# Kernel optimization log

Hardware: AMD Instinct MI355X
Metric: run time of the kernel (lower is better)

The kernel has to match this reference:

```python
import jax, jax.numpy as jnp
import numpy as np

IN = (8, 8, 8, 8)
OUT = (8, 8, 8, 8)
RANK = (1, 16, 16, 16, 1)  # boundary ranks = 1
BATCH = 4096


def setup_inputs() -> dict:
    key = jax.random.key(0)
    ks = jax.random.split(key, 5)
    x = jax.random.normal(ks[0], (BATCH, int(np.prod(IN))), dtype=jnp.float32)
    scale = 0.7  # matches nn.init.uniform_(f, -0.7, 0.7)
    factors = {}
    for k in range(4):
        shp = (RANK[k], OUT[k], IN[k], RANK[k + 1])
        factors[f"f{k}"] = jax.random.uniform(ks[k + 1], shp, jnp.float32, -scale, scale)
    bias = jnp.zeros((int(np.prod(OUT)),), dtype=jnp.float32)  # init.constant_(bias, 0)
    return {"x": x, **factors, "bias": bias}


def reference(x, f0, f1, f2, f3, bias):
    """TT-matrix linear: y = TT(W) @ x_vec + bias, cores of shape (r1, o, i, r2)."""
    cores = [f0, f1, f2, f3]
    B = x.shape[0]
    i0 = cores[0].shape[2]
    # t: (B, A=accumulated out dims, r=current rank, i=current in dim, X=remaining in dims)
    t = x.reshape(B, 1, 1, i0, -1)
    n = len(cores)
    for k, c in enumerate(cores):
        r1, o, i, r2 = c.shape
        # contract current rank and current input mode
        t = jnp.einsum('barix,rois->baosx', t, c)
        A = t.shape[1] * t.shape[2]
        X = t.shape[4]
        if k + 1 < n:
            i_next = cores[k + 1].shape[2]
            t = t.reshape(B, A, r2, i_next, X // i_next)
        else:
            t = t.reshape(B, A)  # r2 == 1, X == 1
    return t + bias
```

## Files before the change

kernel.cpp:

```cpp
#include <hip/hip_runtime.h>

typedef unsigned short u16;
typedef unsigned int u32;
typedef __attribute__((ext_vector_type(8))) short bf16x8;
typedef __attribute__((ext_vector_type(4))) float f32x4;

__device__ __forceinline__ u16 f2bf(float f) {
  u32 u = __float_as_uint(f);
  u += 0x7fffu + ((u >> 16) & 1u);
  return (u16)(u >> 16);
}

__global__ void prep_small(const float* __restrict__ f0, const float* __restrict__ f1,
                           const float* __restrict__ f2, const float* __restrict__ f3,
                           float* __restrict__ W01, float* __restrict__ W23) {
  int b = blockIdx.x;
  if (b < 256) {
    int idx = b * 256 + threadIdx.x;
    int r2 = idx & 15; int t = idx >> 4;
    int i1 = t & 7; t >>= 3;
    int i0 = t & 7; t >>= 3;
    int o1 = t & 7; int o0 = t >> 3;
    const float* a = f0 + (o0 * 8 + i0) * 16;
    const float* c = f1 + (o1 * 8 + i1) * 16 + r2;
    float s = 0.f;
#pragma unroll
    for (int r1 = 0; r1 < 16; ++r1) s += a[r1] * c[r1 * 1024];
    W01[idx] = s;
  } else {
    int idx = (b - 256) * 256 + threadIdx.x;
    int i3 = idx & 7, o3 = (idx >> 3) & 7, i2 = (idx >> 6) & 7;
    int o2 = (idx >> 9) & 7, r2 = idx >> 12;
    const float* a = f2 + ((r2 * 8 + o2) * 8 + i2) * 16;
    const float* c = f3 + o3 * 8 + i3;
    float s = 0.f;
#pragma unroll
    for (int r3 = 0; r3 < 16; ++r3) s += a[r3] * c[r3 * 64];
    W23[idx] = s;
  }
}

__global__ void prep_big(const float* __restrict__ W01, const float* __restrict__ W23,
                         const float* __restrict__ x, u16* __restrict__ W,
                         uint4* __restrict__ xb) {
  int b = blockIdx.x;
  if (b < 8192) {
    int idx = b * 256 + threadIdx.x;
    float4 a = ((const float4*)x)[idx * 2], d = ((const float4*)x)[idx * 2 + 1];
    union { u16 h[8]; uint4 v; } r;
    r.h[0] = f2bf(a.x); r.h[1] = f2bf(a.y); r.h[2] = f2bf(a.z); r.h[3] = f2bf(a.w);
    r.h[4] = f2bf(d.x); r.h[5] = f2bf(d.y); r.h[6] = f2bf(d.z); r.h[7] = f2bf(d.w);
    xb[idx] = r.v;
    return;
  }
  const int o = b - 8192;
  const int o2 = (o >> 3) & 7, o3 = o & 7;
  const int tid = threadIdx.x;
  __shared__ float sW23[1024];

  {
    int e = tid * 4;
    const float* src = W23 + (e >> 6) * 4096 + o2 * 512 + ((e >> 3) & 7) * 64
                         + o3 * 8 + (e & 7);
    ((float4*)sW23)[tid] = *(const float4*)src;
  }
  float w01r[16];
  {
    const float* a = W01 + (((o >> 6) * 64 + (tid >> 2)) << 4);
#pragma unroll
    for (int q = 0; q < 4; ++q) {
      float4 v = *(const float4*)(a + q * 4);
      w01r[q * 4] = v.x; w01r[q * 4 + 1] = v.y; w01r[q * 4 + 2] = v.z; w01r[q * 4 + 3] = v.w;
    }
  }
  __syncthreads();

  const int i2a = 2 * (tid & 3), i2b = i2a + 1;
  float acc[16] = {};
#pragma unroll
  for (int r2 = 0; r2 < 16; ++r2) {
    const float w = w01r[r2];
    const float4 va0 = *(const float4*)(sW23 + r2 * 64 + i2a * 8);
    const float4 va1 = *(const float4*)(sW23 + r2 * 64 + i2a * 8 + 4);
    const float4 vb0 = *(const float4*)(sW23 + r2 * 64 + i2b * 8);
    const float4 vb1 = *(const float4*)(sW23 + r2 * 64 + i2b * 8 + 4);
    acc[0]  += w * va0.x; acc[1]  += w * va0.y; acc[2]  += w * va0.z; acc[3]  += w * va0.w;
    acc[4]  += w * va1.x; acc[5]  += w * va1.y; acc[6]  += w * va1.z; acc[7]  += w * va1.w;
    acc[8]  += w * vb0.x; acc[9]  += w * vb0.y; acc[10] += w * vb0.z; acc[11] += w * vb0.w;
    acc[12] += w * vb1.x; acc[13] += w * vb1.y; acc[14] += w * vb1.z; acc[15] += w * vb1.w;
  }
  union { u16 h[8]; uint4 v; } r0, r1;
#pragma unroll
  for (int j = 0; j < 8; ++j) { r0.h[j] = f2bf(acc[j]); r1.h[j] = f2bf(acc[8 + j]); }
  uint4* dst = (uint4*)(W + (size_t)o * 4096 + tid * 16);
  dst[0] = r0.v; dst[1] = r1.v;
}

__device__ __forceinline__ void gload_lds16(const void* g, void* l) {
  __builtin_amdgcn_global_load_lds((__attribute__((address_space(1))) void*)(g),
                                   (__attribute__((address_space(3))) void*)(l),
                                   16, 0, 0);
}

__global__ __launch_bounds__(512, 2) void gemm256(
    const u16* __restrict__ A, const u16* __restrict__ B,
    const float* __restrict__ bias, float* __restrict__ C) {
  constexpr int K = 4096, N = 4096, NT = 128;
  __shared__ u16 S[65536];
  const int tid  = threadIdx.x;
  const int wave = tid >> 6, lane = tid & 63;
  const int l15 = lane & 15, l4 = lane >> 4;
  const int wr = wave >> 2, wc = wave & 3;
  const int bm = (int)(blockIdx.x >> 4) * 256;
  const int bn = (int)(blockIdx.x & 15) * 256;

  const int rl = tid >> 2;
  const int ls = (tid & 3) ^ ((rl >> 1) & 3);
  const u16* srcA0 = A + (size_t)(bm +       rl) * K + ls * 8;
  const u16* srcA1 = A + (size_t)(bm + 128 + rl) * K + ls * 8;
  const u16* srcB0 = B + (size_t)(bn +       rl) * K + ls * 8;
  const u16* srcB1 = B + (size_t)(bn + 128 + rl) * K + ls * 8;
  const int dA0 = wave * 512,         dA1 = 4096  + wave * 512;
  const int dB0 = 8192 + wave * 512,  dB1 = 12288 + wave * 512;

  int offA[8], offB[4];
#pragma unroll
  for (int mi = 0; mi < 8; ++mi) {
    int r = wr * 128 + mi * 16 + l15;
    offA[mi] = r * 32 + ((l4 ^ ((r >> 1) & 3)) * 8);
  }
#pragma unroll
  for (int ni = 0; ni < 4; ++ni) {
    int r = wc * 64 + ni * 16 + l15;
    offB[ni] = 8192 + r * 32 + ((l4 ^ ((r >> 1) & 3)) * 8);
  }

#define STAGE_A(kts) do { int _s = (kts) & 3; u16* _b = S + _s * 16384;          \
    gload_lds16(srcA0 + (size_t)(kts) * 32, _b + dA0);                           \
    gload_lds16(srcA1 + (size_t)(kts) * 32, _b + dA1); } while (0)
#define STAGE_B(kts) do { int _s = (kts) & 3; u16* _b = S + _s * 16384;          \
    gload_lds16(srcB0 + (size_t)(kts) * 32, _b + dB0);                           \
    gload_lds16(srcB1 + (size_t)(kts) * 32, _b + dB1); } while (0)

  STAGE_A(0); STAGE_B(0);
  STAGE_A(1); STAGE_B(1);
  STAGE_A(2); STAGE_B(2);
  asm volatile("s_waitcnt vmcnt(8)" ::: "memory");
  __builtin_amdgcn_s_barrier();

  f32x4 acc[8][4] = {};

  for (int kt = 0; kt < NT; ++kt) {
    const u16* base = S + (kt & 3) * 16384;
    const int kn = (kt + 3) & (NT - 1);

    bf16x8 av[4], bv[4];
#pragma unroll
    for (int i = 0; i < 4; ++i) av[i] = *(const bf16x8*)(base + offA[i]);
#pragma unroll
    for (int i = 0; i < 4; ++i) bv[i] = *(const bf16x8*)(base + offB[i]);
    STAGE_A(kn);
    __builtin_amdgcn_s_barrier();
    __builtin_amdgcn_s_setprio(1);
#pragma unroll
    for (int mi = 0; mi < 4; ++mi)
#pragma unroll
      for (int ni = 0; ni < 4; ++ni)
        acc[mi][ni] = __builtin_amdgcn_mfma_f32_16x16x32_bf16(
            av[mi], bv[ni], acc[mi][ni], 0, 0, 0);
    __builtin_amdgcn_s_setprio(0);
    __builtin_amdgcn_s_barrier();

#pragma unroll
    for (int i = 0; i < 4; ++i) av[i] = *(const bf16x8*)(base + offA[4 + i]);
    STAGE_B(kn);
    asm volatile("s_waitcnt vmcnt(8)" ::: "memory");
    __builtin_amdgcn_s_barrier();
    __builtin_amdgcn_s_setprio(1);
#pragma unroll
    for (int mi = 0; mi < 4; ++mi)
#pragma unroll
      for (int ni = 0; ni < 4; ++ni)
        acc[4 + mi][ni] = __builtin_amdgcn_mfma_f32_16x16x32_bf16(
            av[mi], bv[ni], acc[4 + mi][ni], 0, 0, 0);
    __builtin_amdgcn_s_setprio(0);
    __builtin_amdgcn_s_barrier();
  }

#pragma unroll
  for (int ni = 0; ni < 4; ++ni) {
    const int col = bn + wc * 64 + ni * 16 + l15;
    const float bvs = bias[col];
#pragma unroll
    for (int mi = 0; mi < 8; ++mi) {
      const int row0 = bm + wr * 128 + mi * 16 + l4 * 4;
#pragma unroll
      for (int j = 0; j < 4; ++j)
        C[(size_t)(row0 + j) * N + col] = acc[mi][ni][j] + bvs;
    }
  }
  asm volatile("s_waitcnt vmcnt(0)" ::: "memory");
#undef STAGE_A
#undef STAGE_B
}

extern "C" void kernel_launch(void* const* d_in, const int* in_sizes, int n_in,
                              void* d_out, int out_size, void* d_ws, size_t ws_size,
                              hipStream_t stream) {
  const float* x    = (const float*)d_in[0];
  const float* f0   = (const float*)d_in[1];
  const float* f1   = (const float*)d_in[2];
  const float* f2   = (const float*)d_in[3];
  const float* f3   = (const float*)d_in[4];
  const float* bias = (const float*)d_in[5];

  char* ws = (char*)d_ws;
  u16* Wb = (u16*)(ws);
  u16* xb = (u16*)(ws + 33554432);
  float* W01 = (float*)d_out;
  float* W23 = (float*)d_out + 65536;

  prep_small<<<512,   256, 0, stream>>>(f0, f1, f2, f3, W01, W23);
  prep_big  <<<12288, 256, 0, stream>>>(W01, W23, x, Wb, (uint4*)xb);
  gemm256   <<<256,   512, 0, stream>>>(xb, Wb, bias, (float*)d_out);
}
```

Measured before the change: 153.9 us.

## Software-pipeline LDS fragment loads across k-tiles in the bf16 GEMM main loop

The GEMM main loop is unrolled by two and uses ping-pong B-fragment registers. The A and B fragments for the next k-tile are read from LDS during the second half of the current tile's MFMAs. This cuts the block barriers per k-tile from four to two and hides LDS read latency behind matrix work. It adds sched_barrier fences around the waitcnt, and the extra fragment registers raise VGPR pressure under launch_bounds(512,2).

```diff
diff --git a/kernel.cpp b/kernel.cpp
--- a/kernel.cpp
+++ b/kernel.cpp
@@ -57,7 +57,6 @@
   const int o2 = (o >> 3) & 7, o3 = o & 7;
   const int tid = threadIdx.x;
   __shared__ float sW23[1024];
-
   {
     int e = tid * 4;
     const float* src = W23 + (e >> 6) * 4096 + o2 * 512 + ((e >> 3) & 7) * 64
@@ -142,49 +141,61 @@
     gload_lds16(srcB0 + (size_t)(kts) * 32, _b + dB0);                           \
     gload_lds16(srcB1 + (size_t)(kts) * 32, _b + dB1); } while (0)
 
+#define ITER(kt, bvU, bvL)                                                       \
+  {                                                                              \
+    const u16* base  = S + ((kt) & 3) * 16384;                                   \
+    const u16* baseN = S + (((kt) + 1) & 3) * 16384;                             \
+    const int kn = ((kt) + 3) & (NT - 1);                                        \
+        \
+    bf16x8 avN[4];                                                               \
+    _Pragma("unroll")                                                            \
+    for (int i = 0; i < 4; ++i) avN[i] = *(const bf16x8*)(base + offA[4 + i]);   \
+    STAGE_A(kn);                                                                 \
+    __builtin_amdgcn_s_setprio(1);                                               \
+    _Pragma("unroll")                                                            \
+    for (int mi = 0; mi < 4; ++mi)                                               \
+      _Pragma("unroll")                                                          \
+      for (int ni = 0; ni < 4; ++ni)                                             \
+        acc[mi][ni] = __builtin_amdgcn_mfma_f32_16x16x32_bf16(                   \
+            avC[mi], bvU[ni], acc[mi][ni], 0, 0, 0);                             \
+    __builtin_amdgcn_s_setprio(0);                                               \
+      \
+    STAGE_B(kn);                                                                 \
+    asm volatile("s_waitcnt vmcnt(8)" ::: "memory");                             \
+    __builtin_amdgcn_sched_barrier(0);                                           \
+    __builtin_amdgcn_s_barrier();                                                \
+    _Pragma("unroll")                                                            \
+    for (int i = 0; i < 4; ++i) avC[i] = *(const bf16x8*)(baseN + offA[i]);      \
+    _Pragma("unroll")                                                            \
+    for (int i = 0; i < 4; ++i) bvL[i] = *(const bf16x8*)(baseN + offB[i]);      \
+    __builtin_amdgcn_s_setprio(1);                                               \
+    _Pragma("unroll")                                                            \
+    for (int mi = 0; mi < 4; ++mi)                                               \
+      _Pragma("unroll")                                                          \
+      for (int ni = 0; ni < 4; ++ni)                                             \
+        acc[4 + mi][ni] = __builtin_amdgcn_mfma_f32_16x16x32_bf16(               \
+            avN[mi], bvU[ni], acc[4 + mi][ni], 0, 0, 0);                         \
+    __builtin_amdgcn_s_setprio(0);                                               \
+    __builtin_amdgcn_s_barrier();                                                \
+  }
+
   STAGE_A(0); STAGE_B(0);
   STAGE_A(1); STAGE_B(1);
   STAGE_A(2); STAGE_B(2);
   asm volatile("s_waitcnt vmcnt(8)" ::: "memory");
+  __builtin_amdgcn_sched_barrier(0);
   __builtin_amdgcn_s_barrier();
 
   f32x4 acc[8][4] = {};
-
-  for (int kt = 0; kt < NT; ++kt) {
-    const u16* base = S + (kt & 3) * 16384;
-    const int kn = (kt + 3) & (NT - 1);
-
-    bf16x8 av[4], bv[4];
-#pragma unroll
-    for (int i = 0; i < 4; ++i) av[i] = *(const bf16x8*)(base + offA[i]);
-#pragma unroll
-    for (int i = 0; i < 4; ++i) bv[i] = *(const bf16x8*)(base + offB[i]);
-    STAGE_A(kn);
-    __builtin_amdgcn_s_barrier();
-    __builtin_amdgcn_s_setprio(1);
-#pragma unroll
-    for (int mi = 0; mi < 4; ++mi)
-#pragma unroll
-      for (int ni = 0; ni < 4; ++ni)
-        acc[mi][ni] = __builtin_amdgcn_mfma_f32_16x16x32_bf16(
-            av[mi], bv[ni], acc[mi][ni], 0, 0, 0);
-    __builtin_amdgcn_s_setprio(0);
-    __builtin_amdgcn_s_barrier();
-
-#pragma unroll
-    for (int i = 0; i < 4; ++i) av[i] = *(const bf16x8*)(base + offA[4 + i]);
-    STAGE_B(kn);
-    asm volatile("s_waitcnt vmcnt(8)" ::: "memory");
-    __builtin_amdgcn_s_barrier();
-    __builtin_amdgcn_s_setprio(1);
-#pragma unroll
-    for (int mi = 0; mi < 4; ++mi)
-#pragma unroll
-      for (int ni = 0; ni < 4; ++ni)
-        acc[4 + mi][ni] = __builtin_amdgcn_mfma_f32_16x16x32_bf16(
-            av[mi], bv[ni], acc[4 + mi][ni], 0, 0, 0);
-    __builtin_amdgcn_s_setprio(0);
-    __builtin_amdgcn_s_barrier();
+  bf16x8 avC[4], bvE[4], bvO[4];
+#pragma unroll
+  for (int i = 0; i < 4; ++i) avC[i] = *(const bf16x8*)(S + offA[i]);
+#pragma unroll
+  for (int i = 0; i < 4; ++i) bvE[i] = *(const bf16x8*)(S + offB[i]);
+
+  for (int kt = 0; kt < NT; kt += 2) {
+    ITER(kt,     bvE, bvO)
+    ITER(kt + 1, bvO, bvE)
   }
 
 #pragma unroll
@@ -202,6 +213,7 @@
   asm volatile("s_waitcnt vmcnt(0)" ::: "memory");
 #undef STAGE_A
 #undef STAGE_B
+#undef ITER
 }
 
 extern "C" void kernel_launch(void* const* d_in, const int* in_sizes, int n_in,
```

Measured after the change: 148.6 us. -3.4%, faster.

## Use 4-wave 128x128 per-wave tiles with register double-buffered LDS fragments

Applied to the files above, without the earlier changes.

The GEMM block drops from 8 waves to 4 waves, and each wave now computes a 128x128 output tile (8x8 MFMA accumulators) instead of 128x64. Each thread issues four staged load groups per k-step. The next k-step's A and B fragments are prefetched from LDS into registers while the current MFMAs run, removing one barrier pair and the setprio toggles. The aim is more MFMA work per LDS read and better overlap of LDS reads with compute. The cost is much higher register pressure (256 accumulator floats per lane) and fewer waves available to hide latency.

```diff
diff --git a/kernel.cpp b/kernel.cpp
--- a/kernel.cpp
+++ b/kernel.cpp
@@ -57,7 +57,6 @@
   const int o2 = (o >> 3) & 7, o3 = o & 7;
   const int tid = threadIdx.x;
   __shared__ float sW23[1024];
-
   {
     int e = tid * 4;
     const float* src = W23 + (e >> 6) * 4096 + o2 * 512 + ((e >> 3) & 7) * 64
@@ -102,7 +101,7 @@
                                    16, 0, 0);
 }
 
-__global__ __launch_bounds__(512, 2) void gemm256(
+__global__ __launch_bounds__(256, 1) void gemm256(
     const u16* __restrict__ A, const u16* __restrict__ B,
     const float* __restrict__ bias, float* __restrict__ C) {
   constexpr int K = 4096, N = 4096, NT = 128;
@@ -110,86 +109,113 @@
   const int tid  = threadIdx.x;
   const int wave = tid >> 6, lane = tid & 63;
   const int l15 = lane & 15, l4 = lane >> 4;
-  const int wr = wave >> 2, wc = wave & 3;
+  const int wr = wave >> 1, wc = wave & 1;
   const int bm = (int)(blockIdx.x >> 4) * 256;
   const int bn = (int)(blockIdx.x & 15) * 256;
 
-  const int rl = tid >> 2;
-  const int ls = (tid & 3) ^ ((rl >> 1) & 3);
-  const u16* srcA0 = A + (size_t)(bm +       rl) * K + ls * 8;
-  const u16* srcA1 = A + (size_t)(bm + 128 + rl) * K + ls * 8;
-  const u16* srcB0 = B + (size_t)(bn +       rl) * K + ls * 8;
-  const u16* srcB1 = B + (size_t)(bn + 128 + rl) * K + ls * 8;
-  const int dA0 = wave * 512,         dA1 = 4096  + wave * 512;
-  const int dB0 = 8192 + wave * 512,  dB1 = 12288 + wave * 512;
-
-  int offA[8], offB[4];
+  const int rg = tid >> 2;
+  const int ls = (tid & 3) ^ ((rg >> 1) & 3);
+  const u16* pA0 = A + (size_t)(bm +       rg) * K + ls * 8;
+  const u16* pA1 = A + (size_t)(bm +  64 + rg) * K + ls * 8;
+  const u16* pA2 = A + (size_t)(bm + 128 + rg) * K + ls * 8;
+  const u16* pA3 = A + (size_t)(bm + 192 + rg) * K + ls * 8;
+  const u16* pB0 = B + (size_t)(bn +       rg) * K + ls * 8;
+  const u16* pB1 = B + (size_t)(bn +  64 + rg) * K + ls * 8;
+  const u16* pB2 = B + (size_t)(bn + 128 + rg) * K + ls * 8;
+  const u16* pB3 = B + (size_t)(bn + 192 + rg) * K + ls * 8;
+  const int dl = tid * 8;
+
+  int offA[8], offB[8];
 #pragma unroll
   for (int mi = 0; mi < 8; ++mi) {
     int r = wr * 128 + mi * 16 + l15;
     offA[mi] = r * 32 + ((l4 ^ ((r >> 1) & 3)) * 8);
   }
 #pragma unroll
-  for (int ni = 0; ni < 4; ++ni) {
-    int r = wc * 64 + ni * 16 + l15;
+  for (int ni = 0; ni < 8; ++ni) {
+    int r = wc * 128 + ni * 16 + l15;
     offB[ni] = 8192 + r * 32 + ((l4 ^ ((r >> 1) & 3)) * 8);
   }
 
-#define STAGE_A(kts) do { int _s = (kts) & 3; u16* _b = S + _s * 16384;          \
-    gload_lds16(srcA0 + (size_t)(kts) * 32, _b + dA0);                           \
-    gload_lds16(srcA1 + (size_t)(kts) * 32, _b + dA1); } while (0)
-#define STAGE_B(kts) do { int _s = (kts) & 3; u16* _b = S + _s * 16384;          \
-    gload_lds16(srcB0 + (size_t)(kts) * 32, _b + dB0);                           \
-    gload_lds16(srcB1 + (size_t)(kts) * 32, _b + dB1); } while (0)
-
-  STAGE_A(0); STAGE_B(0);
-  STAGE_A(1); STAGE_B(1);
-  STAGE_A(2); STAGE_B(2);
-  asm volatile("s_waitcnt vmcnt(8)" ::: "memory");
+#define STG_A01(kts) do { u16* _b = S + ((kts) & 3) * 16384;                     \
+    gload_lds16(pA0 + (size_t)(kts) * 32, _b + dl);                              \
+    gload_lds16(pA1 + (size_t)(kts) * 32, _b + 2048 + dl); } while (0)
+#define STG_A23(kts) do { u16* _b = S + ((kts) & 3) * 16384;                     \
+    gload_lds16(pA2 + (size_t)(kts) * 32, _b + 4096 + dl);                       \
+    gload_lds16(pA3 + (size_t)(kts) * 32, _b + 6144 + dl); } while (0)
+#define STG_B01(kts) do { u16* _b = S + ((kts) & 3) * 16384;                     \
+    gload_lds16(pB0 + (size_t)(kts) * 32, _b + 8192 + dl);                       \
+    gload_lds16(pB1 + (size_t)(kts) * 32, _b + 10240 + dl); } while (0)
+#define STG_B23(kts) do { u16* _b = S + ((kts) & 3) * 16384;                     \
+    gload_lds16(pB2 + (size_t)(kts) * 32, _b + 12288 + dl);                      \
+    gload_lds16(pB3 + (size_t)(kts) * 32, _b + 14336 + dl); } while (0)
+#define STAGE_ALL(kts) do { STG_A01(kts); STG_A23(kts); STG_B01(kts); STG_B23(kts); } while (0)
+
+  STAGE_ALL(0); STAGE_ALL(1); STAGE_ALL(2);
+  asm volatile("s_waitcnt vmcnt(16)" ::: "memory");
+  __builtin_amdgcn_sched_barrier(0);
   __builtin_amdgcn_s_barrier();
 
-  f32x4 acc[8][4] = {};
+  f32x4 acc[8][8] = {};
+  bf16x8 a0[4], a1[4], b0[4], b1[4];
+#pragma unroll
+  for (int i = 0; i < 4; ++i) a0[i] = *(const bf16x8*)(S + offA[i]);
+#pragma unroll
+  for (int i = 0; i < 4; ++i) b0[i] = *(const bf16x8*)(S + offB[i]);
 
   for (int kt = 0; kt < NT; ++kt) {
-    const u16* base = S + (kt & 3) * 16384;
+    const u16* base  = S + (kt & 3) * 16384;
+    const u16* baseN = S + ((kt + 1) & 3) * 16384;
     const int kn = (kt + 3) & (NT - 1);
 
-    bf16x8 av[4], bv[4];
-#pragma unroll
-    for (int i = 0; i < 4; ++i) av[i] = *(const bf16x8*)(base + offA[i]);
-#pragma unroll
-    for (int i = 0; i < 4; ++i) bv[i] = *(const bf16x8*)(base + offB[i]);
-    STAGE_A(kn);
+#pragma unroll
+    for (int i = 0; i < 4; ++i) a1[i] = *(const bf16x8*)(base + offA[4 + i]);
+    STG_A01(kn);
+#pragma unroll
+    for (int mi = 0; mi < 4; ++mi)
+#pragma unroll
+      for (int ni = 0; ni < 4; ++ni)
+        acc[mi][ni] = __builtin_amdgcn_mfma_f32_16x16x32_bf16(
+            a0[mi], b0[ni], acc[mi][ni], 0, 0, 0);
+
+#pragma unroll
+    for (int i = 0; i < 4; ++i) b1[i] = *(const bf16x8*)(base + offB[4 + i]);
+    STG_A23(kn);
+#pragma unroll
+    for (int mi = 0; mi < 4; ++mi)
+#pragma unroll
+      for (int ni = 0; ni < 4; ++ni)
+        acc[4 + mi][ni] = __builtin_amdgcn_mfma_f32_16x16x32_bf16(
+            a1[mi], b0[ni], acc[4 + mi][ni], 0, 0, 0);
+    asm volatile("s_waitcnt vmcnt(12)" ::: "memory");
+    __builtin_amdgcn_sched_barrier(0);
     __builtin_amdgcn_s_barrier();
-    __builtin_amdgcn_s_setprio(1);
-#pragma unroll
-    for (int mi = 0; mi < 4; ++mi)
-#pragma unroll
-      for (int ni = 0; ni < 4; ++ni)
-        acc[mi][ni] = __builtin_amdgcn_mfma_f32_16x16x32_bf16(
-            av[mi], bv[ni], acc[mi][ni], 0, 0, 0);
-    __builtin_amdgcn_s_setprio(0);
+
+#pragma unroll
+    for (int i = 0; i < 4; ++i) b0[i] = *(const bf16x8*)(baseN + offB[i]);
+    STG_B01(kn);
+#pragma unroll
+    for (int mi = 0; mi < 4; ++mi)
+#pragma unroll
+      for (int ni = 0; ni < 4; ++ni)
+        acc[mi][4 + ni] = __builtin_amdgcn_mfma_f32_16x16x32_bf16(
+            a0[mi], b1[ni], acc[mi][4 + ni], 0, 0, 0);
+
+#pragma unroll
+    for (int i = 0; i < 4; ++i) a0[i] = *(const bf16x8*)(baseN + offA[i]);
+    STG_B23(kn);
+#pragma unroll
+    for (int mi = 0; mi < 4; ++mi)
+#pragma unroll
+      for (int ni = 0; ni < 4; ++ni)
+        acc[4 + mi][4 + ni] = __builtin_amdgcn_mfma_f32_16x16x32_bf16(
+            a1[mi], b1[ni], acc[4 + mi][4 + ni], 0, 0, 0);
     __builtin_amdgcn_s_barrier();
-
-#pragma unroll
-    for (int i = 0; i < 4; ++i) av[i] = *(const bf16x8*)(base + offA[4 + i]);
-    STAGE_B(kn);
-    asm volatile("s_waitcnt vmcnt(8)" ::: "memory");
-    __builtin_amdgcn_s_barrier();
-    __builtin_amdgcn_s_setprio(1);
-#pragma unroll
-    for (int mi = 0; mi < 4; ++mi)
-#pragma unroll
-      for (int ni = 0; ni < 4; ++ni)
-        acc[4 + mi][ni] = __builtin_amdgcn_mfma_f32_16x16x32_bf16(
-            av[mi], bv[ni], acc[4 + mi][ni], 0, 0, 0);
-    __builtin_amdgcn_s_setprio(0);
-    __builtin_amdgcn_s_barrier();
-  }
-
-#pragma unroll
-  for (int ni = 0; ni < 4; ++ni) {
-    const int col = bn + wc * 64 + ni * 16 + l15;
+  }
+
+#pragma unroll
+  for (int ni = 0; ni < 8; ++ni) {
+    const int col = bn + wc * 128 + ni * 16 + l15;
     const float bvs = bias[col];
 #pragma unroll
     for (int mi = 0; mi < 8; ++mi) {
@@ -200,8 +226,11 @@
     }
   }
   asm volatile("s_waitcnt vmcnt(0)" ::: "memory");
-#undef STAGE_A
-#undef STAGE_B
+#undef STG_A01
+#undef STG_A23
+#undef STG_B01
+#undef STG_B23
+#undef STAGE_ALL
 }
 
 extern "C" void kernel_launch(void* const* d_in, const int* in_sizes, int n_in,
@@ -222,5 +251,5 @@
 
   prep_small<<<512,   256, 0, stream>>>(f0, f1, f2, f3, W01, W23);
   prep_big  <<<12288, 256, 0, stream>>>(W01, W23, x, Wb, (uint4*)xb);
-  gemm256   <<<256,   512, 0, stream>>>(xb, Wb, bias, (float*)d_out);
-}
+  gemm256   <<<256,   256, 0, stream>>>(xb, Wb, bias, (float*)d_out);
+}
```

Result: slower. 370.9 us (+141.0%).

## Retile GEMM to 256x128 tiles with 4 waves and double-buffered LDS

Applied to the files above, without the earlier changes.

Changes the GEMM block from 512 threads on 256x256 tiles to 256 threads on 256x128 tiles, doubling the grid to 512 blocks. The 4-stage split A/B pipeline becomes a 2-slot double buffer with one combined stage per k-step, and sched_group_barrier hints interleave LDS reads, MFMAs and global loads. It cuts barriers per iteration and shrinks LDS so more blocks can be resident, but it waits on vmcnt(0) every iteration and each block reads more A data relative to its output.

```diff
diff --git a/kernel.cpp b/kernel.cpp
--- a/kernel.cpp
+++ b/kernel.cpp
@@ -57,7 +57,6 @@
   const int o2 = (o >> 3) & 7, o3 = o & 7;
   const int tid = threadIdx.x;
   __shared__ float sW23[1024];
-
   {
     int e = tid * 4;
     const float* src = W23 + (e >> 6) * 4096 + o2 * 512 + ((e >> 3) & 7) * 64
@@ -102,26 +101,27 @@
                                    16, 0, 0);
 }
 
-__global__ __launch_bounds__(512, 2) void gemm256(
+__global__ __launch_bounds__(256, 2) void gemm256(
     const u16* __restrict__ A, const u16* __restrict__ B,
     const float* __restrict__ bias, float* __restrict__ C) {
   constexpr int K = 4096, N = 4096, NT = 128;
-  __shared__ u16 S[65536];
+  __shared__ u16 S[24576];
   const int tid  = threadIdx.x;
   const int wave = tid >> 6, lane = tid & 63;
   const int l15 = lane & 15, l4 = lane >> 4;
-  const int wr = wave >> 2, wc = wave & 3;
-  const int bm = (int)(blockIdx.x >> 4) * 256;
-  const int bn = (int)(blockIdx.x & 15) * 256;
-
-  const int rl = tid >> 2;
-  const int ls = (tid & 3) ^ ((rl >> 1) & 3);
-  const u16* srcA0 = A + (size_t)(bm +       rl) * K + ls * 8;
-  const u16* srcA1 = A + (size_t)(bm + 128 + rl) * K + ls * 8;
-  const u16* srcB0 = B + (size_t)(bn +       rl) * K + ls * 8;
-  const u16* srcB1 = B + (size_t)(bn + 128 + rl) * K + ls * 8;
-  const int dA0 = wave * 512,         dA1 = 4096  + wave * 512;
-  const int dB0 = 8192 + wave * 512,  dB1 = 12288 + wave * 512;
+  const int wr = wave >> 1, wc = wave & 1;
+  const int bm = (int)(blockIdx.x >> 5) * 256;
+  const int bn = (int)(blockIdx.x & 31) * 128;
+
+  const int ls = (tid & 3) ^ ((tid >> 3) & 3);
+  const int rr = tid >> 2;
+  const u16* srcA0 = A + (size_t)(bm +       rr) * K + ls * 8;
+  const u16* srcA1 = A + (size_t)(bm +  64 + rr) * K + ls * 8;
+  const u16* srcA2 = A + (size_t)(bm + 128 + rr) * K + ls * 8;
+  const u16* srcA3 = A + (size_t)(bm + 192 + rr) * K + ls * 8;
+  const u16* srcB0 = B + (size_t)(bn +       rr) * K + ls * 8;
+  const u16* srcB1 = B + (size_t)(bn +  64 + rr) * K + ls * 8;
+  const int d8 = tid * 8;
 
   int offA[8], offB[4];
 #pragma unroll
@@ -135,55 +135,53 @@
     offB[ni] = 8192 + r * 32 + ((l4 ^ ((r >> 1) & 3)) * 8);
   }
 
-#define STAGE_A(kts) do { int _s = (kts) & 3; u16* _b = S + _s * 16384;          \
-    gload_lds16(srcA0 + (size_t)(kts) * 32, _b + dA0);                           \
-    gload_lds16(srcA1 + (size_t)(kts) * 32, _b + dA1); } while (0)
-#define STAGE_B(kts) do { int _s = (kts) & 3; u16* _b = S + _s * 16384;          \
-    gload_lds16(srcB0 + (size_t)(kts) * 32, _b + dB0);                           \
-    gload_lds16(srcB1 + (size_t)(kts) * 32, _b + dB1); } while (0)
-
-  STAGE_A(0); STAGE_B(0);
-  STAGE_A(1); STAGE_B(1);
-  STAGE_A(2); STAGE_B(2);
-  asm volatile("s_waitcnt vmcnt(8)" ::: "memory");
+#define STAGE(kts, slot) do { u16* _b = S + (slot) * 12288;                      \
+    gload_lds16(srcA0 + (size_t)(kts) * 32, _b + d8);                            \
+    gload_lds16(srcA1 + (size_t)(kts) * 32, _b + 2048 + d8);                     \
+    gload_lds16(srcA2 + (size_t)(kts) * 32, _b + 4096 + d8);                     \
+    gload_lds16(srcA3 + (size_t)(kts) * 32, _b + 6144 + d8);                     \
+    gload_lds16(srcB0 + (size_t)(kts) * 32, _b + 8192 + d8);                     \
+    gload_lds16(srcB1 + (size_t)(kts) * 32, _b + 10240 + d8); } while (0)
+
+  STAGE(0, 0);
+  asm volatile("s_waitcnt vmcnt(0)");
   __builtin_amdgcn_s_barrier();
 
   f32x4 acc[8][4] = {};
 
   for (int kt = 0; kt < NT; ++kt) {
-    const u16* base = S + (kt & 3) * 16384;
-    const int kn = (kt + 3) & (NT - 1);
-
-    bf16x8 av[4], bv[4];
-#pragma unroll
-    for (int i = 0; i < 4; ++i) av[i] = *(const bf16x8*)(base + offA[i]);
-#pragma unroll
-    for (int i = 0; i < 4; ++i) bv[i] = *(const bf16x8*)(base + offB[i]);
-    STAGE_A(kn);
-    __builtin_amdgcn_s_barrier();
-    __builtin_amdgcn_s_setprio(1);
+    const u16* base = S + (kt & 1) * 12288;
+
+    bf16x8 av[4], avN[4], bv[4];
+#pragma unroll
+    for (int i = 0; i < 4; ++i) av[i]  = *(const bf16x8*)(base + offA[i]);
+#pragma unroll
+    for (int i = 0; i < 4; ++i) bv[i]  = *(const bf16x8*)(base + offB[i]);
+#pragma unroll
+    for (int i = 0; i < 4; ++i) avN[i] = *(const bf16x8*)(base + offA[4 + i]);
+    STAGE((kt + 1) & (NT - 1), (kt & 1) ^ 1);
+
 #pragma unroll
     for (int mi = 0; mi < 4; ++mi)
 #pragma unroll
       for (int ni = 0; ni < 4; ++ni)
         acc[mi][ni] = __builtin_amdgcn_mfma_f32_16x16x32_bf16(
             av[mi], bv[ni], acc[mi][ni], 0, 0, 0);
-    __builtin_amdgcn_s_setprio(0);
-    __builtin_amdgcn_s_barrier();
-
-#pragma unroll
-    for (int i = 0; i < 4; ++i) av[i] = *(const bf16x8*)(base + offA[4 + i]);
-    STAGE_B(kn);
-    asm volatile("s_waitcnt vmcnt(8)" ::: "memory");
-    __builtin_amdgcn_s_barrier();
-    __builtin_amdgcn_s_setprio(1);
 #pragma unroll
     for (int mi = 0; mi < 4; ++mi)
 #pragma unroll
       for (int ni = 0; ni < 4; ++ni)
         acc[4 + mi][ni] = __builtin_amdgcn_mfma_f32_16x16x32_bf16(
-            av[mi], bv[ni], acc[4 + mi][ni], 0, 0, 0);
-    __builtin_amdgcn_s_setprio(0);
+            avN[mi], bv[ni], acc[4 + mi][ni], 0, 0, 0);
+
+    __builtin_amdgcn_sched_group_barrier(0x100, 8, 0);
+    __builtin_amdgcn_sched_group_barrier(0x008, 4, 0);
+    __builtin_amdgcn_sched_group_barrier(0x100, 4, 0);
+    __builtin_amdgcn_sched_group_barrier(0x008, 4, 0);
+    __builtin_amdgcn_sched_group_barrier(0x070, 6, 0);
+    __builtin_amdgcn_sched_group_barrier(0x008, 24, 0);
+
+    asm volatile("s_waitcnt vmcnt(0)");
     __builtin_amdgcn_s_barrier();
   }
 
@@ -200,8 +198,7 @@
     }
   }
   asm volatile("s_waitcnt vmcnt(0)" ::: "memory");
-#undef STAGE_A
-#undef STAGE_B
+#undef STAGE
 }
 
 extern "C" void kernel_launch(void* const* d_in, const int* in_sizes, int n_in,
@@ -222,5 +219,5 @@
 
   prep_small<<<512,   256, 0, stream>>>(f0, f1, f2, f3, W01, W23);
   prep_big  <<<12288, 256, 0, stream>>>(W01, W23, x, Wb, (uint4*)xb);
-  gemm256   <<<256,   512, 0, stream>>>(xb, Wb, bias, (float*)d_out);
-}
+  gemm256   <<<512,   256, 0, stream>>>(xb, Wb, bias, (float*)d_out);
+}
```

New measurement: 170.9 us. 1.11x slower.
